# Performance work log

Hardware: AMD Instinct MI355X
Metric: run time of the kernel (lower is better)

## Reference

```python
import jax, jax.numpy as jnp
import numpy as np

NEG_INF = -1e30  # stand-in for -inf before softmax (stable under fp16/bf16 too)


def setup_inputs() -> dict:
    key = jax.random.key(0)
    ks = jax.random.split(key, 6)
    B, T, C = 8, 2048, 384
    H, Dh = 6, 64
    s = 0.02
    return {
        "x": jax.random.normal(ks[0], (B, T, C), dtype=jnp.float32),
        "Wq": jax.random.normal(ks[1], (H, C, Dh), dtype=jnp.float32) * s,
        "Wk": jax.random.normal(ks[2], (H, C, Dh), dtype=jnp.float32) * s,
        "Wv": jax.random.normal(ks[3], (H, C, Dh), dtype=jnp.float32) * s,
        "Wp": jax.random.normal(ks[4], (C, C), dtype=jnp.float32) * s,
        "bp": jnp.zeros((C,), dtype=jnp.float32),
    }


def reference(x, Wq, Wk, Wv, Wp, bp):
    # x: [B, T, C]; Wq/Wk/Wv: [H, C, Dh] (per-head independent projections,
    # matching the torch ModuleList of Heads); Wp: [C, C]; bp: [C].
    B, T, C = x.shape
    H, _, Dh = Wq.shape
    scale = Dh ** -0.5  # torch uses self.head_size ** -0.5

    q = jnp.einsum('btc,hcd->bhtd', x, Wq)
    k = jnp.einsum('btc,hcd->bhtd', x, Wk)
    v = jnp.einsum('btc,hcd->bhtd', x, Wv)

    scores = jnp.einsum('bhtd,bhsd->bhts', q, k) * scale  # [B,H,T,T]
    causal = jnp.tril(jnp.ones((T, T), dtype=bool))       # tril mask
    scores = jnp.where(causal, scores, NEG_INF)
    wei = jax.nn.softmax(scores, axis=-1)
    # dropout layers are identity in eval mode

    out = jnp.einsum('bhts,bhsd->bhtd', wei, v)            # [B,H,T,Dh]
    out = out.transpose(0, 2, 1, 3).reshape(B, T, H * Dh)  # concat heads on last dim
    return out @ Wp + bp
```

## Files before the change

kernel.cpp:

```cpp
#include <hip/hip_runtime.h>
#include <hip/hip_bf16.h>

constexpr int T_ = 2048;
constexpr int C_ = 384;
constexpr int H_ = 6;
constexpr int D_ = 64;

typedef unsigned int u32;
typedef unsigned short u16;
typedef __attribute__((ext_vector_type(4))) float f32x4;
typedef __attribute__((ext_vector_type(16))) float f32x16;
typedef __attribute__((ext_vector_type(8))) short bf16x8;
typedef __attribute__((ext_vector_type(4))) short bf16x4;

__device__ __forceinline__ u32 f2bf(float f) {
  u32 u = __float_as_uint(f);
  return (u + 0x7FFFu + ((u >> 16) & 1u)) >> 16;
}
__device__ __forceinline__ u32 pk2(float a, float b) {
  return f2bf(a) | (f2bf(b) << 16);
}
__device__ __forceinline__ u32 pkcvt(float a, float b) {
  __hip_bfloat162 h = __float22bfloat162_rn(float2{a, b});
  return *(u32*)&h;
}
__device__ __forceinline__ void gload16(const u16* g, u16* l) {
  __builtin_amdgcn_global_load_lds(
      (const __attribute__((address_space(1))) u32*)g,
      (__attribute__((address_space(3))) u32*)l, 16, 0, 0);
}

constexpr float SC_ = 0.18033688011112042f;

__global__ __launch_bounds__(256) void xcvt_kernel(
    const float* __restrict__ x, u16* __restrict__ xb) {
  const int id = blockIdx.x * 256 + threadIdx.x;
  const float* s = x + (size_t)id * 8;
  f32x4 a = *(const f32x4*)s, b = *(const f32x4*)(s + 4);
  uint4 o;
  o.x = pkcvt(a[0], a[1]); o.y = pkcvt(a[2], a[3]);
  o.z = pkcvt(b[0], b[1]); o.w = pkcvt(b[2], b[3]);
  *(uint4*)(xb + (size_t)id * 8) = o;
}

__global__ __launch_bounds__(256) void convert_kernel(
    const float* __restrict__ Wq, const float* __restrict__ Wk,
    const float* __restrict__ Wv, const float* __restrict__ Wp,
    u16* __restrict__ Wt, u16* __restrict__ Wpt) {
  int id = blockIdx.x * 256 + threadIdx.x;
  if (id < 110592) {
    int n = id / 96, c0 = (id % 96) * 4;
    int mat = n / 384, nn = n % 384, h = nn >> 6, d = nn & 63;
    const float* W = (mat == 0) ? Wq : ((mat == 1) ? Wk : Wv);
    const float* s = W + (size_t)(h * C_ + c0) * D_ + d;
    uint2 o; o.x = pk2(s[0], s[64]); o.y = pk2(s[128], s[192]);
    *(uint2*)&Wt[(size_t)n * 384 + c0] = o;
  } else {
    int id2 = id - 110592;
    int n = id2 / 96, c0 = (id2 % 96) * 4;
    const float* s = Wp + (size_t)c0 * C_ + n;
    uint2 o; o.x = pk2(s[0], s[384]); o.y = pk2(s[768], s[1152]);
    *(uint2*)&Wpt[(size_t)n * 384 + c0] = o;
  }
}

#define GEMM_BODY(A_PTR, B_PTR)                                                \
  __shared__ u16 As[128 * 64], Bs[128 * 64];                                   \
  const int tid = threadIdx.x;                                                 \
  const int l = tid & 63, w = tid >> 6;                                        \
  const int wr = w >> 1, wc = w & 1;                                           \
  const int ql = l & 15, g = l >> 4;                                           \
  const int rc = l >> 3;                     \
  const int sgr = l & 7;                 \
  f32x4 acc[4][4];                                                             \
  _Pragma("unroll") for (int fi = 0; fi < 4; ++fi)                             \
  _Pragma("unroll") for (int fj = 0; fj < 4; ++fj) acc[fi][fj] = (f32x4)0.f;   \
  for (int kc = 0; kc < 6; ++kc) {                                             \
    if (kc) __syncthreads();                                                   \
    _Pragma("unroll") for (int c = 0; c < 4; ++c) {                            \
      const int rbase = w * 32 + c * 8;                                        \
      const int row = rbase + rc;                                              \
      const int gcol = (sgr ^ (row & 7)) * 8;     \
      gload16((A_PTR) + (size_t)(m0 + row) * 384 + kc * 64 + gcol,             \
              &As[rbase * 64]);                                                \
      gload16((B_PTR) + (size_t)(n0 + row) * 384 + kc * 64 + gcol,             \
              &Bs[rbase * 64]);                                                \
    }                                                                          \
    __syncthreads();                 \
    __builtin_amdgcn_s_setprio(1);                                             \
    _Pragma("unroll") for (int ks = 0; ks < 2; ++ks) {                         \
      bf16x8 af[4], bfr[4];                                                    \
      const int gl = ks * 4 + g;                                               \
      const int slot8 = (gl ^ (ql & 7)) * 8;                                   \
      _Pragma("unroll") for (int fi = 0; fi < 4; ++fi)                         \
        af[fi] = *(const bf16x8*)&As[(wr * 64 + fi * 16 + ql) * 64 + slot8];   \
      _Pragma("unroll") for (int fj = 0; fj < 4; ++fj)                         \
        bfr[fj] = *(const bf16x8*)&Bs[(wc * 64 + fj * 16 + ql) * 64 + slot8];  \
      _Pragma("unroll") for (int fi = 0; fi < 4; ++fi)                         \
      _Pragma("unroll") for (int fj = 0; fj < 4; ++fj)                         \
        acc[fi][fj] = __builtin_amdgcn_mfma_f32_16x16x32_bf16(                 \
            af[fi], bfr[fj], acc[fi][fj], 0, 0, 0);                            \
    }                                                                          \
    __builtin_amdgcn_s_setprio(0);                                             \
  }

__global__ __launch_bounds__(256) void gemm_qkv(
    const u16* __restrict__ xb, const u16* __restrict__ Wt,
    u16* __restrict__ Qb, u16* __restrict__ Kb, u16* __restrict__ Vtb) {
  const int bx = blockIdx.x;
  const int mt = bx / 9, nt = bx % 9;
  const int m0 = mt * 128, n0 = nt * 128;

  GEMM_BODY(xb, Wt)

  const int mat = nt / 3;
#pragma unroll
  for (int fi = 0; fi < 4; ++fi) {
    const int m = m0 + wr * 64 + fi * 16 + g * 4;
    const int b = m >> 11, t = m & 2047;
#pragma unroll
    for (int fj = 0; fj < 4; ++fj) {
      const int n = n0 + wc * 64 + fj * 16 + ql;
      const int nn = n - mat * 384, h = nn >> 6, d = nn & 63;
      if (mat == 0) {
        u16* dst = Qb + ((size_t)(b * H_ + h) * T_ + t) * D_ + d;
#pragma unroll
        for (int r = 0; r < 4; ++r)
          dst[(size_t)r * D_] = (u16)f2bf(acc[fi][fj][r] * SC_);
      } else if (mat == 1) {
        u16* dst = Kb + ((size_t)(b * H_ + h) * T_ + t) * D_ + d;
#pragma unroll
        for (int r = 0; r < 4; ++r) dst[(size_t)r * D_] = (u16)f2bf(acc[fi][fj][r]);
      } else {
        u16* dst = Vtb + ((size_t)(b * H_ + h) * D_ + d) * T_ + t;
        uint2 o;
        o.x = pkcvt(acc[fi][fj][0], acc[fi][fj][1]);
        o.y = pkcvt(acc[fi][fj][2], acc[fi][fj][3]);
        *(uint2*)dst = o;
      }
    }
  }
}

__global__ __launch_bounds__(256) void gemm_proj(
    const u16* __restrict__ attnb, const u16* __restrict__ Wpt,
    const float* __restrict__ bp, float* __restrict__ out) {
  const int bx = blockIdx.x;
  const int mt = bx / 3, nt = bx % 3;
  const int m0 = mt * 128, n0 = nt * 128;

  GEMM_BODY(attnb, Wpt)

#pragma unroll
  for (int fj = 0; fj < 4; ++fj) {
    const int n = n0 + wc * 64 + fj * 16 + ql;
    const float bias = bp[n];
#pragma unroll
    for (int fi = 0; fi < 4; ++fi) {
      const int m = m0 + wr * 64 + fi * 16 + g * 4;
#pragma unroll
      for (int r = 0; r < 4; ++r)
        out[(size_t)(m + r) * C_ + n] = acc[fi][fj][r] + bias;
    }
  }
}

__global__ __launch_bounds__(256) void attn_mfma_kernel(
    const u16* __restrict__ Qb, const u16* __restrict__ Kb,
    const u16* __restrict__ Vtb, u16* __restrict__ attnb) {
  __shared__ u16 Ks[2][64 * 64];
  __shared__ u16 Vs[2][64 * 64];
  const int tid = threadIdx.x;
  const int bx = blockIdx.x;
  const int qb = 15 - (bx / 48);
  const int bh = bx % 48;
  const int h = bh % H_, b = bh / H_;
  const int Q0 = qb * 128;
  const int nt = 2 * qb + 2;
  const size_t hb = (size_t)bh * T_ * D_;

  const int l = tid & 63, w = tid >> 6;
  const int hi = l >> 5, l31 = l & 31;
  const int qw0 = Q0 + w * 32;
  const int qrow = qw0 + l31;
  const int qwmax = qw0 + 31;

  const int srow0 = tid >> 3, sc16 = tid & 7;
  const int srow1 = srow0 + 32;
  const int sw0 = srow0 * 64 + ((sc16 * 8) ^ ((srow0 & 7) * 8));
  const int sw1 = srow1 * 64 + ((sc16 * 8) ^ ((srow1 & 7) * 8));

  bf16x8 qf[4];
  {
    const u16* qg = Qb + hb + (size_t)qrow * D_ + hi * 8;
#pragma unroll
    for (int cs = 0; cs < 4; ++cs) qf[cs] = *(const bf16x8*)(qg + cs * 16);
  }

  {
    uint4 k0 = *(const uint4*)(Kb + hb + (size_t)srow0 * D_ + sc16 * 8);
    uint4 k1 = *(const uint4*)(Kb + hb + (size_t)srow1 * D_ + sc16 * 8);
    uint4 v0 = *(const uint4*)(Vtb + hb + (size_t)srow0 * T_ + sc16 * 8);
    uint4 v1 = *(const uint4*)(Vtb + hb + (size_t)srow1 * T_ + sc16 * 8);
    *(uint4*)&Ks[0][sw0] = k0; *(uint4*)&Ks[0][sw1] = k1;
    *(uint4*)&Vs[0][sw0] = v0; *(uint4*)&Vs[0][sw1] = v1;
  }
  __syncthreads();

  f32x16 oacc[2];
  oacc[0] = (f32x16)0.f; oacc[1] = (f32x16)0.f;
  float lrun = 0.f;
  int cur = 0;
  const int swzA = (l31 & 7) * 8;

  for (int jt = 0; jt < nt; ++jt) {
    const bool have_next = (jt + 1) < nt;
    uint4 kn0, kn1, vn0, vn1;
    if (have_next) {
      const size_t kbase = hb + (size_t)(jt + 1) * 64 * D_;
      kn0 = *(const uint4*)(Kb + kbase + (size_t)srow0 * D_ + sc16 * 8);
      kn1 = *(const uint4*)(Kb + kbase + (size_t)srow1 * D_ + sc16 * 8);
      const size_t vbase = hb + (size_t)(jt + 1) * 64;
      vn0 = *(const uint4*)(Vtb + vbase + (size_t)srow0 * T_ + sc16 * 8);
      vn1 = *(const uint4*)(Vtb + vbase + (size_t)srow1 * T_ + sc16 * 8);
    }

    if (jt * 64 <= qwmax) {
      f32x16 sacc[2];
      sacc[0] = (f32x16)0.f; sacc[1] = (f32x16)0.f;
      __builtin_amdgcn_s_setprio(1);
#pragma unroll
      for (int kc = 0; kc < 2; ++kc) {
#pragma unroll
        for (int cs = 0; cs < 4; ++cs) {
          bf16x8 kf = *(const bf16x8*)
              &Ks[cur][(kc * 32 + l31) * 64 + ((cs * 16 + 8 * hi) ^ swzA)];
          sacc[kc] = __builtin_amdgcn_mfma_f32_32x32x16_bf16(kf, qf[cs], sacc[kc], 0, 0, 0);
        }
      }
      __builtin_amdgcn_s_setprio(0);

      float ps[32];
      if ((jt + 1) * 64 > qw0) {
#pragma unroll
        for (int kc = 0; kc < 2; ++kc)
#pragma unroll
          for (int r = 0; r < 16; ++r) {
            const int kglob = jt * 64 + kc * 32 + (r & 3) + 8 * (r >> 2) + 4 * hi;
            ps[kc * 16 + r] = __builtin_amdgcn_exp2f(
                kglob > qrow ? -1e30f : sacc[kc][r]);
          }
      } else {
#pragma unroll
        for (int kc = 0; kc < 2; ++kc)
#pragma unroll
          for (int r = 0; r < 16; ++r)
            ps[kc * 16 + r] = __builtin_amdgcn_exp2f(sacc[kc][r]);
      }

      float sm[16];
#pragma unroll
      for (int i = 0; i < 16; ++i) sm[i] = ps[i] + ps[i + 16];
#pragma unroll
      for (int i = 0; i < 8; ++i) sm[i] = sm[i] + sm[i + 8];
#pragma unroll
      for (int i = 0; i < 4; ++i) sm[i] = sm[i] + sm[i + 4];
      float rs = (sm[0] + sm[1]) + (sm[2] + sm[3]);
      rs += __shfl_xor(rs, 32);
      lrun += rs;

      u32 pw[4][4];
#pragma unroll
      for (int ks = 0; ks < 4; ++ks)
#pragma unroll
        for (int wd = 0; wd < 4; ++wd)
          pw[ks][wd] = pkcvt(ps[(ks >> 1) * 16 + (ks & 1) * 8 + 2 * wd],
                             ps[(ks >> 1) * 16 + (ks & 1) * 8 + 2 * wd + 1]);

      __builtin_amdgcn_s_setprio(1);
#pragma unroll
      for (int dc = 0; dc < 2; ++dc) {
#pragma unroll
        for (int ks = 0; ks < 4; ++ks) {
          const int rb = (dc * 32 + l31) * 64;
          bf16x4 v0 = *(const bf16x4*)&Vs[cur][rb + ((ks * 16 + 4 * hi) ^ swzA)];
          bf16x4 v1 = *(const bf16x4*)&Vs[cur][rb + ((ks * 16 + 4 * hi + 8) ^ swzA)];
          bf16x8 vf;
          *(bf16x4*)&vf = v0; *((bf16x4*)&vf + 1) = v1;
          bf16x8 pf;
          *(uint4*)&pf = make_uint4(pw[ks][0], pw[ks][1], pw[ks][2], pw[ks][3]);
          oacc[dc] = __builtin_amdgcn_mfma_f32_32x32x16_bf16(vf, pf, oacc[dc], 0, 0, 0);
        }
      }
      __builtin_amdgcn_s_setprio(0);
    }

    __syncthreads();
    if (have_next) {
      *(uint4*)&Ks[cur ^ 1][sw0] = kn0; *(uint4*)&Ks[cur ^ 1][sw1] = kn1;
      *(uint4*)&Vs[cur ^ 1][sw0] = vn0; *(uint4*)&Vs[cur ^ 1][sw1] = vn1;
    }
    __syncthreads();
    cur ^= 1;
  }

  const float inv = 1.0f / lrun;
  u16* obase = attnb + ((size_t)(b * T_ + qrow)) * C_ + h * 64;
#pragma unroll
  for (int dc = 0; dc < 2; ++dc)
#pragma unroll
    for (int g4 = 0; g4 < 4; ++g4) {
      uint2 o;
      o.x = pkcvt(oacc[dc][g4 * 4 + 0] * inv, oacc[dc][g4 * 4 + 1] * inv);
      o.y = pkcvt(oacc[dc][g4 * 4 + 2] * inv, oacc[dc][g4 * 4 + 3] * inv);
      *(uint2*)(obase + dc * 32 + 8 * g4 + 4 * hi) = o;
    }
}

extern "C" void kernel_launch(void* const* d_in, const int* in_sizes, int n_in,
                              void* d_out, int out_size, void* d_ws, size_t ws_size,
                              hipStream_t stream) {
  (void)in_sizes; (void)n_in; (void)out_size; (void)ws_size;
  const float* x  = (const float*)d_in[0];
  const float* Wq = (const float*)d_in[1];
  const float* Wk = (const float*)d_in[2];
  const float* Wv = (const float*)d_in[3];
  const float* Wp = (const float*)d_in[4];
  const float* bp = (const float*)d_in[5];
  float* out = (float*)d_out;

  u16* Wt    = (u16*)d_ws;
  u16* Wpt   = Wt + 442368;
  u16* Qb    = Wpt + 147456;
  u16* Kb    = Qb + 6291456;
  u16* Vtb   = Kb + 6291456;
  u16* R     = Vtb + 6291456;
  u16* xb    = R;
  u16* attnb = R;

  xcvt_kernel<<<3072, 256, 0, stream>>>(x, xb);
  convert_kernel<<<576, 256, 0, stream>>>(Wq, Wk, Wv, Wp, Wt, Wpt);
  gemm_qkv<<<1152, 256, 0, stream>>>(xb, Wt, Qb, Kb, Vtb);
  attn_mfma_kernel<<<768, 256, 0, stream>>>(Qb, Kb, Vtb, attnb);
  gemm_proj<<<384, 256, 0, stream>>>(attnb, Wpt, bp, out);
}
```

Before: 112.3 us.

## Software-pipeline attention loop: overlap next QK^T MFMA with previous tile softmax/PV

Splits the per-tile attention body into an S-phase (QK^T MFMAs) and a finish phase (mask, exp2, row sum, bf16 pack, PV MFMAs). The S-phase of tile jt now runs alongside the finish of tile jt-1, using two ping-ponged score register sets. The intent is to hide exp/VALU work behind matrix-core work. It also adds a min-blocks-per-CU launch bound of 3, which caps registers even though the second score set raises register demand, so spills are a risk.

```diff
diff --git a/kernel.cpp b/kernel.cpp
--- a/kernel.cpp
+++ b/kernel.cpp
@@ -165,7 +165,7 @@
   }
 }
 
-__global__ __launch_bounds__(256) void attn_mfma_kernel(
+__global__ __launch_bounds__(256, 3) void attn_mfma_kernel(
     const u16* __restrict__ Qb, const u16* __restrict__ Kb,
     const u16* __restrict__ Vtb, u16* __restrict__ attnb) {
   __shared__ u16 Ks[2][64 * 64];
@@ -210,99 +210,107 @@
   f32x16 oacc[2];
   oacc[0] = (f32x16)0.f; oacc[1] = (f32x16)0.f;
   float lrun = 0.f;
-  int cur = 0;
   const int swzA = (l31 & 7) * 8;
 
-  for (int jt = 0; jt < nt; ++jt) {
-    const bool have_next = (jt + 1) < nt;
+  auto sphase = [&](f32x16 (&sacc)[2], int jt) {
+    sacc[0] = (f32x16)0.f; sacc[1] = (f32x16)0.f;
+    if (jt * 64 > qwmax) return;
+    const u16* kb = Ks[jt & 1];
+    __builtin_amdgcn_s_setprio(1);
+#pragma unroll
+    for (int kc = 0; kc < 2; ++kc)
+#pragma unroll
+      for (int cs = 0; cs < 4; ++cs) {
+        bf16x8 kf = *(const bf16x8*)
+            &kb[(kc * 32 + l31) * 64 + ((cs * 16 + 8 * hi) ^ swzA)];
+        sacc[kc] = __builtin_amdgcn_mfma_f32_32x32x16_bf16(kf, qf[cs], sacc[kc], 0, 0, 0);
+      }
+    __builtin_amdgcn_s_setprio(0);
+  };
+
+  auto finish = [&](f32x16 (&sacc)[2], int jt) {
+    if (jt * 64 > qwmax) return;
+    if ((jt + 1) * 64 > qw0) {
+#pragma unroll
+      for (int kc = 0; kc < 2; ++kc)
+#pragma unroll
+        for (int r = 0; r < 16; ++r) {
+          const int kglob = jt * 64 + kc * 32 + (r & 3) + 8 * (r >> 2) + 4 * hi;
+          sacc[kc][r] = __builtin_amdgcn_exp2f(
+              kglob > qrow ? -1e30f : sacc[kc][r]);
+        }
+    } else {
+#pragma unroll
+      for (int kc = 0; kc < 2; ++kc)
+#pragma unroll
+        for (int r = 0; r < 16; ++r)
+          sacc[kc][r] = __builtin_amdgcn_exp2f(sacc[kc][r]);
+    }
+    float sm[8];
+#pragma unroll
+    for (int i = 0; i < 8; ++i)
+      sm[i] = (sacc[0][i] + sacc[0][i + 8]) + (sacc[1][i] + sacc[1][i + 8]);
+#pragma unroll
+    for (int i = 0; i < 4; ++i) sm[i] = sm[i] + sm[i + 4];
+    float rs = (sm[0] + sm[1]) + (sm[2] + sm[3]);
+    rs += __shfl_xor(rs, 32);
+    lrun += rs;
+    u32 pw[4][4];
+#pragma unroll
+    for (int ks = 0; ks < 4; ++ks)
+#pragma unroll
+      for (int wd = 0; wd < 4; ++wd)
+        pw[ks][wd] = pkcvt(sacc[ks >> 1][(ks & 1) * 8 + 2 * wd],
+                           sacc[ks >> 1][(ks & 1) * 8 + 2 * wd + 1]);
+    const u16* vb = Vs[jt & 1];
+    __builtin_amdgcn_s_setprio(1);
+#pragma unroll
+    for (int dc = 0; dc < 2; ++dc) {
+#pragma unroll
+      for (int ks = 0; ks < 4; ++ks) {
+        const int rb = (dc * 32 + l31) * 64;
+        bf16x4 v0 = *(const bf16x4*)&vb[rb + ((ks * 16 + 4 * hi) ^ swzA)];
+        bf16x4 v1 = *(const bf16x4*)&vb[rb + ((ks * 16 + 4 * hi + 8) ^ swzA)];
+        bf16x8 vf;
+        *(bf16x4*)&vf = v0; *((bf16x4*)&vf + 1) = v1;
+        bf16x8 pf;
+        *(uint4*)&pf = make_uint4(pw[ks][0], pw[ks][1], pw[ks][2], pw[ks][3]);
+        oacc[dc] = __builtin_amdgcn_mfma_f32_32x32x16_bf16(vf, pf, oacc[dc], 0, 0, 0);
+      }
+    }
+    __builtin_amdgcn_s_setprio(0);
+  };
+
+  auto slot = [&](int jt, f32x16 (&cur)[2], f32x16 (&pend)[2], bool do_fin) {
+    const int tn = jt + 1;
+    const bool have_next = tn < nt;
     uint4 kn0, kn1, vn0, vn1;
     if (have_next) {
-      const size_t kbase = hb + (size_t)(jt + 1) * 64 * D_;
+      const size_t kbase = hb + (size_t)tn * 64 * D_;
       kn0 = *(const uint4*)(Kb + kbase + (size_t)srow0 * D_ + sc16 * 8);
       kn1 = *(const uint4*)(Kb + kbase + (size_t)srow1 * D_ + sc16 * 8);
-      const size_t vbase = hb + (size_t)(jt + 1) * 64;
+      const size_t vbase = hb + (size_t)tn * 64;
       vn0 = *(const uint4*)(Vtb + vbase + (size_t)srow0 * T_ + sc16 * 8);
       vn1 = *(const uint4*)(Vtb + vbase + (size_t)srow1 * T_ + sc16 * 8);
     }
-
-    if (jt * 64 <= qwmax) {
-      f32x16 sacc[2];
-      sacc[0] = (f32x16)0.f; sacc[1] = (f32x16)0.f;
-      __builtin_amdgcn_s_setprio(1);
-#pragma unroll
-      for (int kc = 0; kc < 2; ++kc) {
-#pragma unroll
-        for (int cs = 0; cs < 4; ++cs) {
-          bf16x8 kf = *(const bf16x8*)
-              &Ks[cur][(kc * 32 + l31) * 64 + ((cs * 16 + 8 * hi) ^ swzA)];
-          sacc[kc] = __builtin_amdgcn_mfma_f32_32x32x16_bf16(kf, qf[cs], sacc[kc], 0, 0, 0);
-        }
-      }
-      __builtin_amdgcn_s_setprio(0);
-
-      float ps[32];
-      if ((jt + 1) * 64 > qw0) {
-#pragma unroll
-        for (int kc = 0; kc < 2; ++kc)
-#pragma unroll
-          for (int r = 0; r < 16; ++r) {
-            const int kglob = jt * 64 + kc * 32 + (r & 3) + 8 * (r >> 2) + 4 * hi;
-            ps[kc * 16 + r] = __builtin_amdgcn_exp2f(
-                kglob > qrow ? -1e30f : sacc[kc][r]);
-          }
-      } else {
-#pragma unroll
-        for (int kc = 0; kc < 2; ++kc)
-#pragma unroll
-          for (int r = 0; r < 16; ++r)
-            ps[kc * 16 + r] = __builtin_amdgcn_exp2f(sacc[kc][r]);
-      }
-
-      float sm[16];
-#pragma unroll
-      for (int i = 0; i < 16; ++i) sm[i] = ps[i] + ps[i + 16];
-#pragma unroll
-      for (int i = 0; i < 8; ++i) sm[i] = sm[i] + sm[i + 8];
-#pragma unroll
-      for (int i = 0; i < 4; ++i) sm[i] = sm[i] + sm[i + 4];
-      float rs = (sm[0] + sm[1]) + (sm[2] + sm[3]);
-      rs += __shfl_xor(rs, 32);
-      lrun += rs;
-
-      u32 pw[4][4];
-#pragma unroll
-      for (int ks = 0; ks < 4; ++ks)
-#pragma unroll
-        for (int wd = 0; wd < 4; ++wd)
-          pw[ks][wd] = pkcvt(ps[(ks >> 1) * 16 + (ks & 1) * 8 + 2 * wd],
-                             ps[(ks >> 1) * 16 + (ks & 1) * 8 + 2 * wd + 1]);
-
-      __builtin_amdgcn_s_setprio(1);
-#pragma unroll
-      for (int dc = 0; dc < 2; ++dc) {
-#pragma unroll
-        for (int ks = 0; ks < 4; ++ks) {
-          const int rb = (dc * 32 + l31) * 64;
-          bf16x4 v0 = *(const bf16x4*)&Vs[cur][rb + ((ks * 16 + 4 * hi) ^ swzA)];
-          bf16x4 v1 = *(const bf16x4*)&Vs[cur][rb + ((ks * 16 + 4 * hi + 8) ^ swzA)];
-          bf16x8 vf;
-          *(bf16x4*)&vf = v0; *((bf16x4*)&vf + 1) = v1;
-          bf16x8 pf;
-          *(uint4*)&pf = make_uint4(pw[ks][0], pw[ks][1], pw[ks][2], pw[ks][3]);
-          oacc[dc] = __builtin_amdgcn_mfma_f32_32x32x16_bf16(vf, pf, oacc[dc], 0, 0, 0);
-        }
-      }
-      __builtin_amdgcn_s_setprio(0);
-    }
-
+    sphase(cur, jt);
+    if (do_fin) finish(pend, jt - 1);
     __syncthreads();
     if (have_next) {
-      *(uint4*)&Ks[cur ^ 1][sw0] = kn0; *(uint4*)&Ks[cur ^ 1][sw1] = kn1;
-      *(uint4*)&Vs[cur ^ 1][sw0] = vn0; *(uint4*)&Vs[cur ^ 1][sw1] = vn1;
+      const int nb = tn & 1;
+      *(uint4*)&Ks[nb][sw0] = kn0; *(uint4*)&Ks[nb][sw1] = kn1;
+      *(uint4*)&Vs[nb][sw0] = vn0; *(uint4*)&Vs[nb][sw1] = vn1;
     }
     __syncthreads();
-    cur ^= 1;
-  }
+  };
+
+  f32x16 sA[2], sB[2];
+  slot(0, sA, sB, false);
+  for (int p = 1; p < nt; p += 2) {
+    slot(p, sB, sA, true);
+    if (p + 1 < nt) slot(p + 1, sA, sB, true);
+  }
+  finish(sB, nt - 1);
 
   const float inv = 1.0f / lrun;
   u16* obase = attnb + ((size_t)(b * T_ + qrow)) * C_ + h * 64;
```

New measurement: 217.5 us. 93.7% more time.

## Software-pipeline P·V MFMA of previous tile with current tile's softmax

Applied to the files above, without the earlier changes.

Restructures the attention inner loop so the P·V matrix multiply for key tile jt-1 is issued after the QK^T MFMAs of tile jt and before that tile's exp and packing. The intent is to let the VALU exp/sum/convert work overlap with matrix-core work instead of running them strictly in sequence. Packed probabilities are carried across iterations in registers, exp results are written in place into the score accumulators, and one P·V step is drained after the loop. This raises register pressure and relies on the shared-memory V buffer for the previous tile staying intact until the next barrier.

```diff
diff --git a/kernel.cpp b/kernel.cpp
--- a/kernel.cpp
+++ b/kernel.cpp
@@ -165,6 +165,24 @@
   }
 }
 
+#define OFMA(VB)                                                               \
+  do {                                                                         \
+    __builtin_amdgcn_s_setprio(1);                                             \
+    _Pragma("unroll") for (int dc = 0; dc < 2; ++dc) {                         \
+      _Pragma("unroll") for (int ks = 0; ks < 4; ++ks) {                       \
+        const int rb = (dc * 32 + l31) * 64;                                   \
+        bf16x4 v0 = *(const bf16x4*)&(VB)[rb + ((ks * 16 + 4 * hi) ^ swzA)];   \
+        bf16x4 v1 = *(const bf16x4*)&(VB)[rb + ((ks * 16 + 4 * hi + 8) ^ swzA)]; \
+        bf16x8 vf;                                                             \
+        *(bf16x4*)&vf = v0; *((bf16x4*)&vf + 1) = v1;                          \
+        bf16x8 pf;                                                             \
+        *(uint4*)&pf = make_uint4(pwP[ks][0], pwP[ks][1], pwP[ks][2], pwP[ks][3]); \
+        oacc[dc] = __builtin_amdgcn_mfma_f32_32x32x16_bf16(vf, pf, oacc[dc], 0, 0, 0); \
+      }                                                                        \
+    }                                                                          \
+    __builtin_amdgcn_s_setprio(0);                                             \
+  } while (0)
+
 __global__ __launch_bounds__(256) void attn_mfma_kernel(
     const u16* __restrict__ Qb, const u16* __restrict__ Kb,
     const u16* __restrict__ Vtb, u16* __restrict__ attnb) {
@@ -210,7 +228,7 @@
   f32x16 oacc[2];
   oacc[0] = (f32x16)0.f; oacc[1] = (f32x16)0.f;
   float lrun = 0.f;
-  int cur = 0;
+  u32 pwP[4][4];
   const int swzA = (l31 & 7) * 8;
 
   for (int jt = 0; jt < nt; ++jt) {
@@ -225,29 +243,38 @@
       vn1 = *(const uint4*)(Vtb + vbase + (size_t)srow1 * T_ + sc16 * 8);
     }
 
-    if (jt * 64 <= qwmax) {
-      f32x16 sacc[2];
-      sacc[0] = (f32x16)0.f; sacc[1] = (f32x16)0.f;
+    const bool active = jt * 64 <= qwmax;
+    const bool prev_active = (jt >= 1) && ((jt - 1) * 64 <= qwmax);
+
+    f32x16 sacc[2];
+    sacc[0] = (f32x16)0.f; sacc[1] = (f32x16)0.f;
+    if (active) {
+      const u16* kb = Ks[jt & 1];
       __builtin_amdgcn_s_setprio(1);
 #pragma unroll
-      for (int kc = 0; kc < 2; ++kc) {
+      for (int kc = 0; kc < 2; ++kc)
 #pragma unroll
         for (int cs = 0; cs < 4; ++cs) {
           bf16x8 kf = *(const bf16x8*)
-              &Ks[cur][(kc * 32 + l31) * 64 + ((cs * 16 + 8 * hi) ^ swzA)];
+              &kb[(kc * 32 + l31) * 64 + ((cs * 16 + 8 * hi) ^ swzA)];
           sacc[kc] = __builtin_amdgcn_mfma_f32_32x32x16_bf16(kf, qf[cs], sacc[kc], 0, 0, 0);
         }
-      }
       __builtin_amdgcn_s_setprio(0);
-
-      float ps[32];
+    }
+
+    if (prev_active) {
+      const u16* vb = Vs[(jt & 1) ^ 1];
+      OFMA(vb);
+    }
+
+    if (active) {
       if ((jt + 1) * 64 > qw0) {
 #pragma unroll
         for (int kc = 0; kc < 2; ++kc)
 #pragma unroll
           for (int r = 0; r < 16; ++r) {
             const int kglob = jt * 64 + kc * 32 + (r & 3) + 8 * (r >> 2) + 4 * hi;
-            ps[kc * 16 + r] = __builtin_amdgcn_exp2f(
+            sacc[kc][r] = __builtin_amdgcn_exp2f(
                 kglob > qrow ? -1e30f : sacc[kc][r]);
           }
       } else {
@@ -255,53 +282,37 @@
         for (int kc = 0; kc < 2; ++kc)
 #pragma unroll
           for (int r = 0; r < 16; ++r)
-            ps[kc * 16 + r] = __builtin_amdgcn_exp2f(sacc[kc][r]);
+            sacc[kc][r] = __builtin_amdgcn_exp2f(sacc[kc][r]);
       }
-
-      float sm[16];
-#pragma unroll
-      for (int i = 0; i < 16; ++i) sm[i] = ps[i] + ps[i + 16];
-#pragma unroll
-      for (int i = 0; i < 8; ++i) sm[i] = sm[i] + sm[i + 8];
+      float sm[8];
+#pragma unroll
+      for (int i = 0; i < 8; ++i)
+        sm[i] = (sacc[0][i] + sacc[0][i + 8]) + (sacc[1][i] + sacc[1][i + 8]);
 #pragma unroll
       for (int i = 0; i < 4; ++i) sm[i] = sm[i] + sm[i + 4];
       float rs = (sm[0] + sm[1]) + (sm[2] + sm[3]);
       rs += __shfl_xor(rs, 32);
       lrun += rs;
-
-      u32 pw[4][4];
 #pragma unroll
       for (int ks = 0; ks < 4; ++ks)
 #pragma unroll
         for (int wd = 0; wd < 4; ++wd)
-          pw[ks][wd] = pkcvt(ps[(ks >> 1) * 16 + (ks & 1) * 8 + 2 * wd],
-                             ps[(ks >> 1) * 16 + (ks & 1) * 8 + 2 * wd + 1]);
-
-      __builtin_amdgcn_s_setprio(1);
-#pragma unroll
-      for (int dc = 0; dc < 2; ++dc) {
-#pragma unroll
-        for (int ks = 0; ks < 4; ++ks) {
-          const int rb = (dc * 32 + l31) * 64;
-          bf16x4 v0 = *(const bf16x4*)&Vs[cur][rb + ((ks * 16 + 4 * hi) ^ swzA)];
-          bf16x4 v1 = *(const bf16x4*)&Vs[cur][rb + ((ks * 16 + 4 * hi + 8) ^ swzA)];
-          bf16x8 vf;
-          *(bf16x4*)&vf = v0; *((bf16x4*)&vf + 1) = v1;
-          bf16x8 pf;
-          *(uint4*)&pf = make_uint4(pw[ks][0], pw[ks][1], pw[ks][2], pw[ks][3]);
-          oacc[dc] = __builtin_amdgcn_mfma_f32_32x32x16_bf16(vf, pf, oacc[dc], 0, 0, 0);
-        }
-      }
-      __builtin_amdgcn_s_setprio(0);
+          pwP[ks][wd] = pkcvt(sacc[ks >> 1][(ks & 1) * 8 + 2 * wd],
+                              sacc[ks >> 1][(ks & 1) * 8 + 2 * wd + 1]);
     }
 
     __syncthreads();
     if (have_next) {
-      *(uint4*)&Ks[cur ^ 1][sw0] = kn0; *(uint4*)&Ks[cur ^ 1][sw1] = kn1;
-      *(uint4*)&Vs[cur ^ 1][sw0] = vn0; *(uint4*)&Vs[cur ^ 1][sw1] = vn1;
+      const int nb = (jt + 1) & 1;
+      *(uint4*)&Ks[nb][sw0] = kn0; *(uint4*)&Ks[nb][sw1] = kn1;
+      *(uint4*)&Vs[nb][sw0] = vn0; *(uint4*)&Vs[nb][sw1] = vn1;
     }
     __syncthreads();
-    cur ^= 1;
+  }
+
+  if ((nt - 1) * 64 <= qwmax) {
+    const u16* vb = Vs[(nt - 1) & 1];
+    OFMA(vb);
   }
 
   const float inv = 1.0f / lrun;
```

Measured after the change: 114.1 us. About the same (+1.6%).

## Load K/V tiles directly from global into LDS and drop one barrier

Applied to the files above, without the earlier changes.

K and V tiles now reach shared memory through a direct global-to-LDS load helper (gload16), with the XOR swizzle applied to the source column. The previous path staged them in registers and wrote them to LDS after the compute. The per-tile prefetch writes straight into the alternate buffer, so each loop iteration needs one barrier instead of two. The goal is to cut VGPR pressure and LDS-store instructions and to overlap loads with the MFMA work. Correctness depends on the single barrier also waiting for the outstanding direct loads before the buffer is read.

```diff
diff --git a/kernel.cpp b/kernel.cpp
--- a/kernel.cpp
+++ b/kernel.cpp
@@ -184,11 +184,8 @@
   const int qw0 = Q0 + w * 32;
   const int qrow = qw0 + l31;
   const int qwmax = qw0 + 31;
-
-  const int srow0 = tid >> 3, sc16 = tid & 7;
-  const int srow1 = srow0 + 32;
-  const int sw0 = srow0 * 64 + ((sc16 * 8) ^ ((srow0 & 7) * 8));
-  const int sw1 = srow1 * 64 + ((sc16 * 8) ^ ((srow1 & 7) * 8));
+  const int rc = l >> 3;
+  const int sgr = l & 7;
 
   bf16x8 qf[4];
   {
@@ -197,32 +194,35 @@
     for (int cs = 0; cs < 4; ++cs) qf[cs] = *(const bf16x8*)(qg + cs * 16);
   }
 
-  {
-    uint4 k0 = *(const uint4*)(Kb + hb + (size_t)srow0 * D_ + sc16 * 8);
-    uint4 k1 = *(const uint4*)(Kb + hb + (size_t)srow1 * D_ + sc16 * 8);
-    uint4 v0 = *(const uint4*)(Vtb + hb + (size_t)srow0 * T_ + sc16 * 8);
-    uint4 v1 = *(const uint4*)(Vtb + hb + (size_t)srow1 * T_ + sc16 * 8);
-    *(uint4*)&Ks[0][sw0] = k0; *(uint4*)&Ks[0][sw1] = k1;
-    *(uint4*)&Vs[0][sw0] = v0; *(uint4*)&Vs[0][sw1] = v1;
+#pragma unroll
+  for (int c = 0; c < 2; ++c) {
+    const int rbase = w * 16 + c * 8;
+    const int row = rbase + rc;
+    const int gc = (sgr ^ (row & 7)) * 8;
+    gload16(Kb + hb + (size_t)row * D_ + gc, &Ks[0][rbase * 64]);
+    gload16(Vtb + hb + (size_t)row * T_ + gc, &Vs[0][rbase * 64]);
   }
   __syncthreads();
 
   f32x16 oacc[2];
   oacc[0] = (f32x16)0.f; oacc[1] = (f32x16)0.f;
   float lrun = 0.f;
-  int cur = 0;
   const int swzA = (l31 & 7) * 8;
 
   for (int jt = 0; jt < nt; ++jt) {
-    const bool have_next = (jt + 1) < nt;
-    uint4 kn0, kn1, vn0, vn1;
-    if (have_next) {
-      const size_t kbase = hb + (size_t)(jt + 1) * 64 * D_;
-      kn0 = *(const uint4*)(Kb + kbase + (size_t)srow0 * D_ + sc16 * 8);
-      kn1 = *(const uint4*)(Kb + kbase + (size_t)srow1 * D_ + sc16 * 8);
-      const size_t vbase = hb + (size_t)(jt + 1) * 64;
-      vn0 = *(const uint4*)(Vtb + vbase + (size_t)srow0 * T_ + sc16 * 8);
-      vn1 = *(const uint4*)(Vtb + vbase + (size_t)srow1 * T_ + sc16 * 8);
+    const int cur = jt & 1;
+    if (jt + 1 < nt) {
+      const int nb = cur ^ 1;
+#pragma unroll
+      for (int c = 0; c < 2; ++c) {
+        const int rbase = w * 16 + c * 8;
+        const int row = rbase + rc;
+        const int gc = (sgr ^ (row & 7)) * 8;
+        gload16(Kb + hb + (size_t)((jt + 1) * 64 + row) * D_ + gc,
+                &Ks[nb][rbase * 64]);
+        gload16(Vtb + hb + (size_t)row * T_ + (jt + 1) * 64 + gc,
+                &Vs[nb][rbase * 64]);
+      }
     }
 
     if (jt * 64 <= qwmax) {
@@ -230,14 +230,13 @@
       sacc[0] = (f32x16)0.f; sacc[1] = (f32x16)0.f;
       __builtin_amdgcn_s_setprio(1);
 #pragma unroll
-      for (int kc = 0; kc < 2; ++kc) {
+      for (int kc = 0; kc < 2; ++kc)
 #pragma unroll
         for (int cs = 0; cs < 4; ++cs) {
           bf16x8 kf = *(const bf16x8*)
               &Ks[cur][(kc * 32 + l31) * 64 + ((cs * 16 + 8 * hi) ^ swzA)];
           sacc[kc] = __builtin_amdgcn_mfma_f32_32x32x16_bf16(kf, qf[cs], sacc[kc], 0, 0, 0);
         }
-      }
       __builtin_amdgcn_s_setprio(0);
 
       float ps[32];
@@ -296,12 +295,6 @@
     }
 
     __syncthreads();
-    if (have_next) {
-      *(uint4*)&Ks[cur ^ 1][sw0] = kn0; *(uint4*)&Ks[cur ^ 1][sw1] = kn1;
-      *(uint4*)&Vs[cur ^ 1][sw0] = vn0; *(uint4*)&Vs[cur ^ 1][sw1] = vn1;
-    }
-    __syncthreads();
-    cur ^= 1;
   }
 
   const float inv = 1.0f / lrun;
```

Result: no change. 112.4 us (+0.1%).
